# Kernel optimization log

Measured on AMD Instinct MI355X. Metric: run time of the kernel, lower is better.

The kernel has to match this reference:

```python
import jax, jax.numpy as jnp
import numpy as np
import math

B, L, H, E = 16, 1024, 8, 64   # L = nsensor = N (forced by einsum 'bhls,bhlg')
WIN = 1024                      # win_size, last dim of x
G = 64                          # n_group
D_SEL = 1                       # d_sel default


def setup_inputs() -> dict:
    key = jax.random.key(0)
    ks = jax.random.split(key, 7)
    return {
        "queries": jax.random.normal(ks[0], (B, L, H, E), dtype=jnp.float32),
        "keys": jax.random.normal(ks[1], (B, L, H, E), dtype=jnp.float32),
        "values": jax.random.normal(ks[2], (B, L, H, E), dtype=jnp.float32),
        "x": jax.random.normal(ks[3], (B, L, WIN), dtype=jnp.float32),
        "mlp_w": jax.random.normal(ks[4], (H * D_SEL, WIN), dtype=jnp.float32) * 0.02,
        "mlp_b": jax.random.normal(ks[5], (H * D_SEL,), dtype=jnp.float32) * 0.02,
        "sel_W": jax.random.normal(ks[6], (H, G, D_SEL), dtype=jnp.float32),
        "attn_mask": 0,
    }


def _select_attention(x, mlp_w, mlp_b, sel_W, n_heads, d_sel):
    b, n, lwin = x.shape
    xf = x.reshape(b * n, lwin)
    newx = jnp.tanh(xf @ mlp_w.T + mlp_b)                 # [(B*N), H*d_sel]
    # Faithful raw reshape (torch.reshape, no permute): mixes n and h axes.
    newx = newx.reshape(b, n_heads, n, d_sel)             # [B, H, N, d_sel]
    sel = jnp.einsum('bhnd,hgd->bhng', newx, sel_W)       # [B, H, N, G]
    return jax.nn.relu(sel)


def reference(queries, keys, values, x, mlp_w, mlp_b, sel_W, attn_mask):
    b, l, h, e = queries.shape
    scale = 1.0 / math.sqrt(e)
    scores = jnp.einsum('blhe,bshe->bhls', queries, keys)      # [B, H, L, S]
    sel = _select_attention(x, mlp_w, mlp_b, sel_W, h, D_SEL)  # [B, H, L, G]
    scores = jnp.einsum('bhls,bhlg->bhsg', scores, sel)        # [B, H, S, G]
    series = jax.nn.softmax(scale * scores, axis=-1)           # softmax over groups
    # values labeled 'blhs': l=S (value len), s=D (feature). Output V: [B, D, H, G]
    V = jnp.einsum('blhs,bhlg->bshg', values, series)
    return V
```

## Files before the change

kernel.cpp:

```cpp
#include <hip/hip_runtime.h>
#include <math.h>

#define NB 16
#define NL 1024
#define NH 8
#define NE 64
#define NWIN 1024
#define NG 64

#define SCH 64
#define SROW 72
#define NCH 16

typedef __attribute__((ext_vector_type(8))) short short8;
typedef __attribute__((ext_vector_type(4))) float floatx4;

__device__ __forceinline__ short f2bf(float x) {
    unsigned u = __float_as_uint(x);
    u += 0x7fffu + ((u >> 16) & 1u);
    return (short)(u >> 16);
}
__device__ __forceinline__ float dot4(float4 a, float4 b) {
    return fmaf(a.x, b.x, fmaf(a.y, b.y, fmaf(a.z, b.z, a.w * b.w)));
}

__global__ __launch_bounds__(256) void k_sel_q(
    const float* __restrict__ x, const float* __restrict__ mlp_w,
    const float* __restrict__ mlp_b, const float* __restrict__ q,
    float* __restrict__ qp, float* __restrict__ qn)
{
    __shared__ float4 w_lds[8][NWIN / 4];
    __shared__ float t_lds[128];
    __shared__ float redp[4][64], redn[4][64];

    int tid = threadIdx.x;
    int blk = blockIdx.x;
    int h = blk & 7;
    int qq = (blk >> 3) & 7;
    int b = blk >> 6;
    int bh = b * 8 + h;
    int w = tid >> 6, lane = tid & 63;

    const float4* w4 = (const float4*)mlp_w;
    float4* wl = (float4*)w_lds;
    #pragma unroll
    for (int i = 0; i < 8; ++i)
        wl[tid + 256 * i] = w4[tid + 256 * i];
    __syncthreads();

    int r0 = b * 1024 + h * 128 + qq * 16 + w * 4;
    float bc = mlp_b[lane & 7];
    float4 xa[4], xb[4];
    {
        const float4* p0 = (const float4*)(x + (size_t)r0 * NWIN);
        #pragma unroll
        for (int it = 0; it < 4; ++it) xa[it] = p0[it * 64 + lane];
    }
    #pragma unroll
    for (int j = 0; j < 4; ++j) {
        if (j < 3) {
            const float4* pn = (const float4*)(x + (size_t)(r0 + j + 1) * NWIN);
            #pragma unroll
            for (int it = 0; it < 4; ++it) xb[it] = pn[it * 64 + lane];
        }
        float o0=0,o1=0,o2=0,o3=0,o4=0,o5=0,o6=0,o7=0;
        #pragma unroll
        for (int it = 0; it < 4; ++it) {
            float4 xv = xa[it];
            o0 += dot4(xv, w_lds[0][it * 64 + lane]);
            o1 += dot4(xv, w_lds[1][it * 64 + lane]);
            o2 += dot4(xv, w_lds[2][it * 64 + lane]);
            o3 += dot4(xv, w_lds[3][it * 64 + lane]);
            o4 += dot4(xv, w_lds[4][it * 64 + lane]);
            o5 += dot4(xv, w_lds[5][it * 64 + lane]);
            o6 += dot4(xv, w_lds[6][it * 64 + lane]);
            o7 += dot4(xv, w_lds[7][it * 64 + lane]);
        }
        o0 += __shfl_xor(o0, 1, 64); o1 += __shfl_xor(o1, 1, 64);
        o2 += __shfl_xor(o2, 1, 64); o3 += __shfl_xor(o3, 1, 64);
        o4 += __shfl_xor(o4, 1, 64); o5 += __shfl_xor(o5, 1, 64);
        o6 += __shfl_xor(o6, 1, 64); o7 += __shfl_xor(o7, 1, 64);
        bool b0 = lane & 1;
        float m0 = b0 ? o1 : o0, m1 = b0 ? o3 : o2;
        float m2 = b0 ? o5 : o4, m3 = b0 ? o7 : o6;
        m0 += __shfl_xor(m0, 2, 64); m1 += __shfl_xor(m1, 2, 64);
        m2 += __shfl_xor(m2, 2, 64); m3 += __shfl_xor(m3, 2, 64);
        bool b1 = lane & 2;
        float n0 = b1 ? m1 : m0, n1 = b1 ? m3 : m2;
        n0 += __shfl_xor(n0, 4, 64); n1 += __shfl_xor(n1, 4, 64);
        float q0 = (lane & 4) ? n1 : n0;
        q0 += __shfl_xor(q0, 8, 64);
        q0 += __shfl_xor(q0, 16, 64);
        q0 += __shfl_xor(q0, 32, 64);
        if (lane < 8)
            t_lds[w * 32 + j * 8 + lane] = tanhf(q0 + bc);
        #pragma unroll
        for (int it = 0; it < 4; ++it) xa[it] = xb[it];
    }

    int lo = lane >> 4, e4 = lane & 15;
    float4 accp = make_float4(0,0,0,0), accn = make_float4(0,0,0,0);
    #pragma unroll
    for (int i = 0; i < 8; ++i) {
        int l_loc = w * 32 + i * 4 + lo;
        float tv = t_lds[l_loc];
        int l = qq * 128 + l_loc;
        float4 qv = *(const float4*)(q + (((size_t)(b * NL + l)) * NH + h) * NE + e4 * 4);
        float tp = fmaxf(tv, 0.f), tn = fminf(tv, 0.f);
        accp.x = fmaf(tp, qv.x, accp.x); accp.y = fmaf(tp, qv.y, accp.y);
        accp.z = fmaf(tp, qv.z, accp.z); accp.w = fmaf(tp, qv.w, accp.w);
        accn.x = fmaf(tn, qv.x, accn.x); accn.y = fmaf(tn, qv.y, accn.y);
        accn.z = fmaf(tn, qv.z, accn.z); accn.w = fmaf(tn, qv.w, accn.w);
    }
    #pragma unroll
    for (int off = 16; off <= 32; off <<= 1) {
        accp.x += __shfl_xor(accp.x, off, 64); accp.y += __shfl_xor(accp.y, off, 64);
        accp.z += __shfl_xor(accp.z, off, 64); accp.w += __shfl_xor(accp.w, off, 64);
        accn.x += __shfl_xor(accn.x, off, 64); accn.y += __shfl_xor(accn.y, off, 64);
        accn.z += __shfl_xor(accn.z, off, 64); accn.w += __shfl_xor(accn.w, off, 64);
    }
    if (lo == 0) {
        *(float4*)&redp[w][e4 * 4] = accp;
        *(float4*)&redn[w][e4 * 4] = accn;
    }
    __syncthreads();
    if (tid < 64) {
        atomicAdd(&qp[bh * NE + tid], redp[0][tid] + redp[1][tid] + redp[2][tid] + redp[3][tid]);
    } else if (tid < 128) {
        int e = tid - 64;
        atomicAdd(&qn[bh * NE + e], redn[0][e] + redn[1][e] + redn[2][e] + redn[3][e]);
    }
}

__global__ __launch_bounds__(256) void k_attn_out(
    const float* __restrict__ keys, const float* __restrict__ values,
    const float* __restrict__ sel_W,
    const float* __restrict__ qp, const float* __restrict__ qn,
    float* __restrict__ partial)
{
    __shared__ short sb[NG][SROW];
    __shared__ float ap_l[SCH], an_l[SCH];
    __shared__ float2 wpn[NG];
    __shared__ float mx4[4][SCH], dn4[4][SCH];

    int tid = threadIdx.x, blk = blockIdx.x;
    int h = blk & 7;
    int chunk = (blk >> 3) & (NCH - 1);
    int b = blk >> 7;
    int bh = b * 8 + h;
    int w = tid >> 6, lane = tid & 63;
    int c = lane & 15, sq = lane >> 4;
    const float scale = 0.125f;
    int s0 = chunk * SCH;

    float vt[16];
    const float* vbase = values + (((size_t)(b * NL + s0)) * NH + h) * NE + 16 * w + c;
    #pragma unroll
    for (int ks = 0; ks < 2; ++ks)
        #pragma unroll
        for (int j = 0; j < 8; ++j)
            vt[ks * 8 + j] = vbase[(size_t)(ks * 32 + sq * 8 + j) * (NH * NE)];
    float4 k4[4];
    #pragma unroll
    for (int p = 0; p < 4; ++p) {
        int sl = w * 16 + p * 4 + sq;
        k4[p] = *(const float4*)(keys + (((size_t)(b * NL + s0 + sl)) * NH + h) * NE + c * 4);
    }
    __builtin_amdgcn_sched_barrier(0);

    if (tid < NG) {
        float W = sel_W[h * NG + tid];
        wpn[tid] = make_float2(fmaxf(W, 0.f) * scale, fminf(W, 0.f) * scale);
    }
    const float4 qp4 = *(const float4*)(qp + bh * NE + c * 4);
    const float4 qn4 = *(const float4*)(qn + bh * NE + c * 4);

    #pragma unroll
    for (int p = 0; p < 4; ++p) {
        int sl = w * 16 + p * 4 + sq;
        float pp = dot4(k4[p], qp4);
        float pn = dot4(k4[p], qn4);
        #pragma unroll
        for (int m_ = 1; m_ <= 8; m_ <<= 1) {
            pp += __shfl_xor(pp, m_, 64);
            pn += __shfl_xor(pn, m_, 64);
        }
        if (c == 0) { ap_l[sl] = pp; an_l[sl] = pn; }
    }
    __syncthreads();

    {
        int s_ = tid & 63, q4i = tid >> 6, g0 = q4i * 16;
        float ap = ap_l[s_], an = an_l[s_];
        float m = -1e30f;
        #pragma unroll
        for (int g = 0; g < 16; ++g) {
            float2 wv = wpn[g0 + g];
            m = fmaxf(m, fmaf(wv.x, ap, wv.y * an));
        }
        mx4[q4i][s_] = m;
        __syncthreads();
        m = fmaxf(fmaxf(mx4[0][s_], mx4[1][s_]), fmaxf(mx4[2][s_], mx4[3][s_]));
        float d = 0.f;
        #pragma unroll
        for (int g = 0; g < 16; ++g) {
            float2 wv = wpn[g0 + g];
            d += __expf(fmaf(wv.x, ap, wv.y * an) - m);
        }
        dn4[q4i][s_] = d;
        __syncthreads();
        float inv = 1.0f / (dn4[0][s_] + dn4[1][s_] + dn4[2][s_] + dn4[3][s_]);
        #pragma unroll
        for (int g = 0; g < 16; ++g) {
            float2 wv = wpn[g0 + g];
            sb[g0 + g][s_] = f2bf(__expf(fmaf(wv.x, ap, wv.y * an) - m) * inv);
        }
    }
    __syncthreads();

    floatx4 acc[4] = {{0.f,0.f,0.f,0.f},{0.f,0.f,0.f,0.f},
                      {0.f,0.f,0.f,0.f},{0.f,0.f,0.f,0.f}};
    #pragma unroll
    for (int ks = 0; ks < 2; ++ks) {
        short8 av;
        #pragma unroll
        for (int j = 0; j < 8; ++j) av[j] = f2bf(vt[ks * 8 + j]);
        #pragma unroll
        for (int n = 0; n < 4; ++n) {
            short8 bv = *(const short8*)&sb[16 * n + c][ks * 32 + sq * 8];
            acc[n] = __builtin_amdgcn_mfma_f32_16x16x32_bf16(av, bv, acc[n], 0, 0, 0);
        }
    }

    float* pch = partial + (size_t)chunk * (NB * NE * NH * NG);
    #pragma unroll
    for (int n = 0; n < 4; ++n) {
        #pragma unroll
        for (int r = 0; r < 4; ++r) {
            int e = 16 * w + sq * 4 + r;
            int g = 16 * n + c;
            pch[((size_t)(b * NE + e) * NH + h) * NG + g] = acc[n][r];
        }
    }
}

__global__ __launch_bounds__(256) void k_reduce(
    const float* __restrict__ partial, float* __restrict__ out)
{
    int i = blockIdx.x * 256 + threadIdx.x;
    const float4* p = (const float4*)partial;
    float4 s = p[i];
    #pragma unroll
    for (int ch = 1; ch < NCH; ++ch) {
        float4 t = p[(size_t)ch * 131072 + i];
        s.x += t.x; s.y += t.y; s.z += t.z; s.w += t.w;
    }
    ((float4*)out)[i] = s;
}

extern "C" void kernel_launch(void* const* d_in, const int* in_sizes, int n_in,
                              void* d_out, int out_size, void* d_ws, size_t ws_size,
                              hipStream_t stream) {
    (void)in_sizes; (void)n_in; (void)ws_size; (void)out_size;
    const float* queries = (const float*)d_in[0];
    const float* keys    = (const float*)d_in[1];
    const float* values  = (const float*)d_in[2];
    const float* x       = (const float*)d_in[3];
    const float* mlp_w   = (const float*)d_in[4];
    const float* mlp_b   = (const float*)d_in[5];
    const float* sel_W   = (const float*)d_in[6];
    float* out = (float*)d_out;

    float* partial = (float*)d_ws;
    float* qp_ws = partial + (size_t)NCH * (NB * NE * NH * NG);
    float* qn_ws = qp_ws + NB * NH * NE;

    hipMemsetAsync(qp_ws, 0, (size_t)2 * NB * NH * NE * sizeof(float), stream);

    k_sel_q<<<dim3(NB * NH * 8), dim3(256), 0, stream>>>(x, mlp_w, mlp_b,
                                                          queries, qp_ws, qn_ws);
    k_attn_out<<<dim3(NB * NH * NCH), dim3(256), 0, stream>>>(keys, values, sel_W,
                                                              qp_ws, qn_ws, partial);
    k_reduce<<<dim3(512), dim3(256), 0, stream>>>(partial, out);
}
```

Baseline: 201.3 us.

## Compute selector MLP with bf16 MFMA and cut sel_q grid to two blocks per head

Replaces the fp32 dot-product and shuffle-reduction MLP in k_sel_q with a bf16 16x16x32 MFMA over x rows, keeping mlp_w in LDS as padded bf16. Each block now handles 64 rows of x and 512 query rows instead of 16 and 128, so the grid shrinks 4x and the weight load is amortised over more rows. The aim is to cut ALU and shuffle cost in the tanh projection. In exchange it adds bf16 rounding on x and the weights, leaves half the MFMA B columns idle, and gives fewer blocks to hide the latency of the memory-bound 64 MB read of x.

```diff
diff --git a/kernel.cpp b/kernel.cpp
--- a/kernel.cpp
+++ b/kernel.cpp
@@ -11,8 +11,10 @@
 #define SCH 64
 #define SROW 72
 #define NCH 16
+#define PADW 1032
 
 typedef __attribute__((ext_vector_type(8))) short short8;
+typedef __attribute__((ext_vector_type(4))) short short4v;
 typedef __attribute__((ext_vector_type(4))) float floatx4;
 
 __device__ __forceinline__ short f2bf(float x) {
@@ -29,82 +31,68 @@
     const float* __restrict__ mlp_b, const float* __restrict__ q,
     float* __restrict__ qp, float* __restrict__ qn)
 {
-    __shared__ float4 w_lds[8][NWIN / 4];
-    __shared__ float t_lds[128];
+    __shared__ short wb[8][PADW];
+    __shared__ float t_lds[512];
     __shared__ float redp[4][64], redn[4][64];
 
-    int tid = threadIdx.x;
-    int blk = blockIdx.x;
-    int h = blk & 7;
-    int qq = (blk >> 3) & 7;
-    int b = blk >> 6;
+    int tid = threadIdx.x, blk = blockIdx.x;
+    int half = blk & 1, h = (blk >> 1) & 7, b = blk >> 4;
     int bh = b * 8 + h;
     int w = tid >> 6, lane = tid & 63;
-
-    const float4* w4 = (const float4*)mlp_w;
-    float4* wl = (float4*)w_lds;
-    #pragma unroll
-    for (int i = 0; i < 8; ++i)
-        wl[tid + 256 * i] = w4[tid + 256 * i];
-    __syncthreads();
-
-    int r0 = b * 1024 + h * 128 + qq * 16 + w * 4;
-    float bc = mlp_b[lane & 7];
-    float4 xa[4], xb[4];
+    int c = lane & 15, qd = lane >> 4;
+
     {
-        const float4* p0 = (const float4*)(x + (size_t)r0 * NWIN);
-        #pragma unroll
-        for (int it = 0; it < 4; ++it) xa[it] = p0[it * 64 + lane];
-    }
-    #pragma unroll
-    for (int j = 0; j < 4; ++j) {
-        if (j < 3) {
-            const float4* pn = (const float4*)(x + (size_t)(r0 + j + 1) * NWIN);
-            #pragma unroll
-            for (int it = 0; it < 4; ++it) xb[it] = pn[it * 64 + lane];
-        }
-        float o0=0,o1=0,o2=0,o3=0,o4=0,o5=0,o6=0,o7=0;
-        #pragma unroll
-        for (int it = 0; it < 4; ++it) {
-            float4 xv = xa[it];
-            o0 += dot4(xv, w_lds[0][it * 64 + lane]);
-            o1 += dot4(xv, w_lds[1][it * 64 + lane]);
-            o2 += dot4(xv, w_lds[2][it * 64 + lane]);
-            o3 += dot4(xv, w_lds[3][it * 64 + lane]);
-            o4 += dot4(xv, w_lds[4][it * 64 + lane]);
-            o5 += dot4(xv, w_lds[5][it * 64 + lane]);
-            o6 += dot4(xv, w_lds[6][it * 64 + lane]);
-            o7 += dot4(xv, w_lds[7][it * 64 + lane]);
-        }
-        o0 += __shfl_xor(o0, 1, 64); o1 += __shfl_xor(o1, 1, 64);
-        o2 += __shfl_xor(o2, 1, 64); o3 += __shfl_xor(o3, 1, 64);
-        o4 += __shfl_xor(o4, 1, 64); o5 += __shfl_xor(o5, 1, 64);
-        o6 += __shfl_xor(o6, 1, 64); o7 += __shfl_xor(o7, 1, 64);
-        bool b0 = lane & 1;
-        float m0 = b0 ? o1 : o0, m1 = b0 ? o3 : o2;
-        float m2 = b0 ? o5 : o4, m3 = b0 ? o7 : o6;
-        m0 += __shfl_xor(m0, 2, 64); m1 += __shfl_xor(m1, 2, 64);
-        m2 += __shfl_xor(m2, 2, 64); m3 += __shfl_xor(m3, 2, 64);
-        bool b1 = lane & 2;
-        float n0 = b1 ? m1 : m0, n1 = b1 ? m3 : m2;
-        n0 += __shfl_xor(n0, 4, 64); n1 += __shfl_xor(n1, 4, 64);
-        float q0 = (lane & 4) ? n1 : n0;
-        q0 += __shfl_xor(q0, 8, 64);
-        q0 += __shfl_xor(q0, 16, 64);
-        q0 += __shfl_xor(q0, 32, 64);
-        if (lane < 8)
-            t_lds[w * 32 + j * 8 + lane] = tanhf(q0 + bc);
-        #pragma unroll
-        for (int it = 0; it < 4; ++it) xa[it] = xb[it];
-    }
+        int row = tid >> 5;
+        int seg = tid & 31;
+        const float4* src = (const float4*)(mlp_w + (size_t)row * NWIN + seg * 32);
+        #pragma unroll
+        for (int i = 0; i < 8; ++i) {
+            float4 v = src[i];
+            short4v s4 = {f2bf(v.x), f2bf(v.y), f2bf(v.z), f2bf(v.w)};
+            *(short4v*)&wb[row][seg * 32 + i * 4] = s4;
+        }
+    }
+    __syncthreads();
+
+    int rw = b * 1024 + h * 128 + half * 64 + w * 16;
+    const float* xrow = x + (size_t)(rw + c) * NWIN + qd * 8;
+    floatx4 acc = {0.f, 0.f, 0.f, 0.f};
+    float4 a0a = *(const float4*)(xrow);
+    float4 a0b = *(const float4*)(xrow + 4);
+    #pragma unroll 8
+    for (int ks = 0; ks < 32; ++ks) {
+        float4 a1a, a1b;
+        if (ks < 31) {
+            a1a = *(const float4*)(xrow + (ks + 1) * 32);
+            a1b = *(const float4*)(xrow + (ks + 1) * 32 + 4);
+        }
+        short8 av;
+        av[0] = f2bf(a0a.x); av[1] = f2bf(a0a.y);
+        av[2] = f2bf(a0a.z); av[3] = f2bf(a0a.w);
+        av[4] = f2bf(a0b.x); av[5] = f2bf(a0b.y);
+        av[6] = f2bf(a0b.z); av[7] = f2bf(a0b.w);
+        short8 bv = {0,0,0,0,0,0,0,0};
+        if (c < 8) bv = *(const short8*)&wb[c][ks * 32 + qd * 8];
+        acc = __builtin_amdgcn_mfma_f32_16x16x32_bf16(av, bv, acc, 0, 0, 0);
+        a0a = a1a; a0b = a1b;
+    }
+    if (c < 8) {
+        float bias = mlp_b[c];
+        #pragma unroll
+        for (int r = 0; r < 4; ++r) {
+            int l8 = w * 16 + qd * 4 + r;
+            t_lds[l8 * 8 + c] = tanhf(acc[r] + bias);
+        }
+    }
+    __syncthreads();
 
     int lo = lane >> 4, e4 = lane & 15;
     float4 accp = make_float4(0,0,0,0), accn = make_float4(0,0,0,0);
-    #pragma unroll
-    for (int i = 0; i < 8; ++i) {
-        int l_loc = w * 32 + i * 4 + lo;
+    #pragma unroll 4
+    for (int i = 0; i < 32; ++i) {
+        int l_loc = w * 128 + i * 4 + lo;
         float tv = t_lds[l_loc];
-        int l = qq * 128 + l_loc;
+        int l = half * 512 + l_loc;
         float4 qv = *(const float4*)(q + (((size_t)(b * NL + l)) * NH + h) * NE + e4 * 4);
         float tp = fmaxf(tv, 0.f), tn = fminf(tv, 0.f);
         accp.x = fmaf(tp, qv.x, accp.x); accp.y = fmaf(tp, qv.y, accp.y);
@@ -277,7 +265,7 @@
 
     hipMemsetAsync(qp_ws, 0, (size_t)2 * NB * NH * NE * sizeof(float), stream);
 
-    k_sel_q<<<dim3(NB * NH * 8), dim3(256), 0, stream>>>(x, mlp_w, mlp_b,
+    k_sel_q<<<dim3(NB * NH * 2), dim3(256), 0, stream>>>(x, mlp_w, mlp_b,
                                                           queries, qp_ws, qn_ws);
     k_attn_out<<<dim3(NB * NH * NCH), dim3(256), 0, stream>>>(keys, values, sel_W,
                                                               qp_ws, qn_ws, partial);
```

Measured after the change: 204.1 us. No clear change (+1.4%).
